# Optimization experiments

Measured on AMD Instinct MI355X. Metric: run time of the kernel, lower is better.

Reference implementation:

```python
import jax, jax.numpy as jnp
import numpy as np

B, T, H, D = 512, 256, 256, 3  # batch, seq_len, RNN_hid_dim, var_dim


def setup_inputs() -> dict:
    key = jax.random.key(0)
    ks = jax.random.split(key, 14)
    s = 1.0 / np.sqrt(H)  # PyTorch GRU init scale
    return {
        "X_p": jax.random.normal(ks[0], (B, T, D), jnp.float32),
        "X_f": jax.random.normal(ks[1], (B, T, D), jnp.float32),
        "noise": jax.random.normal(ks[2], (1, B, H), jnp.float32),
        # encoder GRU params (PyTorch layout: gates ordered r, z, n)
        "W_ih_enc": jax.random.uniform(ks[3], (3 * H, D), jnp.float32, -s, s),
        "W_hh_enc": jax.random.uniform(ks[4], (3 * H, H), jnp.float32, -s, s),
        "b_ih_enc": jax.random.uniform(ks[5], (3 * H,), jnp.float32, -s, s),
        "b_hh_enc": jax.random.uniform(ks[6], (3 * H,), jnp.float32, -s, s),
        # decoder GRU params
        "W_ih_dec": jax.random.uniform(ks[7], (3 * H, D), jnp.float32, -s, s),
        "W_hh_dec": jax.random.uniform(ks[8], (3 * H, H), jnp.float32, -s, s),
        "b_ih_dec": jax.random.uniform(ks[9], (3 * H,), jnp.float32, -s, s),
        "b_hh_dec": jax.random.uniform(ks[10], (3 * H,), jnp.float32, -s, s),
        # output projection
        "W_fc": jax.random.uniform(ks[11], (D, H), jnp.float32, -s, s),
        "b_fc": jax.random.uniform(ks[12], (D,), jnp.float32, -s, s),
    }


def _gru(x, h0, W_ih, W_hh, b_ih, b_hh):
    # x: [B, T, D]; h0: [B, H]. PyTorch GRU cell math, gate order r, z, n.
    xg = jnp.einsum('btd,gd->btg', x, W_ih) + b_ih  # [B, T, 3H] (one big GEMM)

    def step(h, xg_t):
        gh = h @ W_hh.T + b_hh                      # [B, 3H]
        xr, xz, xn = jnp.split(xg_t, 3, axis=-1)
        hr, hz, hn = jnp.split(gh, 3, axis=-1)
        r = jax.nn.sigmoid(xr + hr)
        z = jax.nn.sigmoid(xz + hz)
        n = jnp.tanh(xn + r * hn)
        h_new = (1.0 - z) * n + z * h
        return h_new, h_new

    hT, ys = jax.lax.scan(step, h0, jnp.swapaxes(xg, 0, 1))  # scan over T
    return jnp.swapaxes(ys, 0, 1), hT  # [B, T, H], [B, H]


def reference(X_p, X_f, noise, W_ih_enc, W_hh_enc, b_ih_enc, b_hh_enc,
              W_ih_dec, W_hh_dec, b_ih_dec, b_hh_dec, W_fc, b_fc):
    h0 = jnp.zeros((X_p.shape[0], W_hh_enc.shape[1]), X_p.dtype)
    _, h_t = _gru(X_p, h0, W_ih_enc, W_hh_enc, b_ih_enc, b_hh_enc)
    hidden = h_t + noise[0]                                   # h_t: [B,H], noise: [1,B,H]
    # shift right by one timestep, zero-fill first step
    X_f_shft = jnp.concatenate(
        [jnp.zeros_like(X_f[:, :1, :]), X_f[:, :-1, :]], axis=1)
    Y_f, _ = _gru(X_f_shft, hidden, W_ih_dec, W_hh_dec, b_ih_dec, b_hh_dec)
    return jnp.einsum('bth,dh->btd', Y_f, W_fc) + b_fc        # [B, T, D]
```

## Files before the change

### kernel.cpp

```cpp
#include <hip/hip_runtime.h>


#define B_TOT 512
#define T_LEN 256
#define HID 256
#define NBATCH 16
#define NTHREADS 1024
#define NBLK 32

#define WR_OFF 0
#define H_OFF  32768
#define X_OFF  40960
#define SMEM_SHORTS 57408
#define SMEM_BYTES  (SMEM_SHORTS * 2)

#define XT 64
#define XSLOTS (T_LEN + 1)
#define HBUF (NBATCH * HID)

typedef __attribute__((ext_vector_type(4))) float f32x4;
typedef __attribute__((ext_vector_type(8))) short shortx8;
typedef __attribute__((ext_vector_type(4))) short i16x4;
typedef __attribute__((ext_vector_type(4))) unsigned short ushortx4;
typedef __attribute__((ext_vector_type(8))) unsigned short ushortx8;

#if __has_builtin(__builtin_amdgcn_mfma_f32_16x16x16_bf16)
#define HAVE_K16 1
#define MFMA_X(A, B, C) __builtin_amdgcn_mfma_f32_16x16x16_bf16((A), (B), (C), 0, 0, 0)
#elif __has_builtin(__builtin_amdgcn_mfma_f32_16x16x16bf16_1k)
#define HAVE_K16 1
#define MFMA_X(A, B, C) __builtin_amdgcn_mfma_f32_16x16x16bf16_1k((A), (B), (C), 0, 0, 0)
#else
#define HAVE_K16 0
#endif

__device__ __forceinline__ unsigned short f2bf(float x) {
    unsigned u = __float_as_uint(x);
    u += 0x7FFF + ((u >> 16) & 1);
    return (unsigned short)(u >> 16);
}
__device__ __forceinline__ float bf2f(unsigned short s) {
    return __uint_as_float(((unsigned)s) << 16);
}
__device__ __forceinline__ float fastrcp(float x) {
#if __has_builtin(__builtin_amdgcn_rcpf)
    return __builtin_amdgcn_rcpf(x);
#else
    return 1.0f / x;
#endif
}
__device__ __forceinline__ float exp2raw(float y) {
#if __has_builtin(__builtin_amdgcn_exp2f)
    return __builtin_amdgcn_exp2f(y);
#else
    return __expf(y * 0.69314718056f);
#endif
}
__device__ __forceinline__ float sigmoid_(float x) {
    return fastrcp(1.0f + exp2raw(x * -1.44269504f));
}
__device__ __forceinline__ float tanh_(float x) {
    return 2.0f * fastrcp(1.0f + exp2raw(x * -2.88539008f)) - 1.0f;
}

__global__ __launch_bounds__(256) void prep_wr(
    const float* __restrict__ Whh_enc, const float* __restrict__ Whh_dec,
    unsigned short* __restrict__ wr_enc, unsigned short* __restrict__ wr_dec)
{
    int idx = blockIdx.x * 256 + threadIdx.x;
    int gru = idx >> 12;
    int rem = idx & 4095;
    int lane = rem & 63;
    int kk = (rem >> 6) & 3;
    int ht = rem >> 8;
    const float* W = gru ? Whh_dec : Whh_enc;
    unsigned short* dst = gru ? wr_dec : wr_enc;
    int row = ht * 16 + (lane & 15);
    int col = (kk + 4) * 32 + (lane >> 4) * 8;
    const float* src = W + (size_t)row * 256 + col;
    ushortx8 v;
    #pragma unroll
    for (int j = 0; j < 8; ++j) v[j] = f2bf(src[j]);
    *(ushortx8*)(dst + (size_t)rem * 8) = v;
}

template<int IS_DEC>
__global__ __launch_bounds__(NTHREADS, 4) void gru_persistent(
    const float* __restrict__ X,
    const float* __restrict__ W_hh,
    const float* __restrict__ W_ih,
    const float* __restrict__ b_ih,
    const float* __restrict__ b_hh,
    const unsigned short* __restrict__ Wr4,
    const float* __restrict__ h_in,
    const float* __restrict__ noise,
    float* __restrict__ h_out,
    unsigned short* __restrict__ Yout)
{
    extern __shared__ unsigned short smem[];
    unsigned short* shWr = smem + WR_OFF;
    unsigned short* shH  = smem + H_OFF;
    unsigned short* shX  = smem + X_OFF;

    const int tid  = threadIdx.x;
    const int g    = blockIdx.x;
    const int w    = tid >> 6;
    const int lane = tid & 63;
    const int c    = lane & 15;
    const int q    = lane >> 4;
    const int ht   = w;

    for (int idx = tid; idx < NBATCH * XSLOTS; idx += NTHREADS) {
        int t = idx >> 4, cc = idx & 15;
        int ts = IS_DEC ? (t - 1) : t;
        float x0 = 0.0f, x1 = 0.0f, x2 = 0.0f;
        if (ts >= 0 && ts < T_LEN) {
            const float* xp = X + ((size_t)(g * NBATCH + cc) * T_LEN + ts) * 3;
            x0 = xp[0]; x1 = xp[1]; x2 = xp[2];
        }
        ushortx4 v = {f2bf(x0), f2bf(x1), f2bf(x2), (unsigned short)0x3F80};
        *(ushortx4*)&shX[t * XT + cc * 4] = v;
    }

    {
        int row = ht * 16 + c;
        const float* wp = W_hh + (size_t)row * 256 + q * 8;
        #pragma unroll
        for (int k = 0; k < 4; ++k) {
            const f32x4* p = (const f32x4*)(wp + k * 32);
            f32x4 f0 = p[0];
            f32x4 f1 = p[1];
            shortx8 a;
            a[0] = (short)f2bf(f0[0]); a[1] = (short)f2bf(f0[1]);
            a[2] = (short)f2bf(f0[2]); a[3] = (short)f2bf(f0[3]);
            a[4] = (short)f2bf(f1[0]); a[5] = (short)f2bf(f1[1]);
            a[6] = (short)f2bf(f1[2]); a[7] = (short)f2bf(f1[3]);
            *(shortx8*)&shWr[((ht * 4 + k) * 64 + lane) * 8] = a;
        }
    }

    shortx8 Wf[2][8];
    #pragma unroll
    for (int gg = 0; gg < 2; ++gg) {
        int row = (gg + 1) * 256 + ht * 16 + c;
        const float* wp = W_hh + (size_t)row * 256 + q * 8;
        #pragma unroll
        for (int k = 0; k < 8; ++k) {
            const f32x4* p = (const f32x4*)(wp + k * 32);
            f32x4 f0 = p[0];
            f32x4 f1 = p[1];
            shortx8 a;
            a[0] = (short)f2bf(f0[0]); a[1] = (short)f2bf(f0[1]);
            a[2] = (short)f2bf(f0[2]); a[3] = (short)f2bf(f0[3]);
            a[4] = (short)f2bf(f1[0]); a[5] = (short)f2bf(f1[1]);
            a[6] = (short)f2bf(f1[2]); a[7] = (short)f2bf(f1[3]);
            Wf[gg][k] = a;
        }
    }

#if HAVE_K16
    i16x4 ax[3];
#else
    shortx8 ax[3];
#endif
    {
        int rr_ = ht * 16 + c;
        int rowr = rr_, rowz = 256 + rr_, rown = 512 + rr_;
        short r0 = 0, r1 = 0, r2 = 0, r3 = 0, z0 = 0, z1 = 0, z2 = 0, z3 = 0;
        short n0 = 0, n1 = 0, n2 = 0, n3 = 0;
        if (q == 0) {
            r0 = (short)f2bf(W_ih[rowr * 3 + 0]);
            r1 = (short)f2bf(W_ih[rowr * 3 + 1]);
            r2 = (short)f2bf(W_ih[rowr * 3 + 2]);
            r3 = (short)f2bf(b_ih[rowr] + b_hh[rowr]);
            z0 = (short)f2bf(W_ih[rowz * 3 + 0]);
            z1 = (short)f2bf(W_ih[rowz * 3 + 1]);
            z2 = (short)f2bf(W_ih[rowz * 3 + 2]);
            z3 = (short)f2bf(b_ih[rowz] + b_hh[rowz]);
            n0 = (short)f2bf(W_ih[rown * 3 + 0]);
            n1 = (short)f2bf(W_ih[rown * 3 + 1]);
            n2 = (short)f2bf(W_ih[rown * 3 + 2]);
            n3 = (short)f2bf(b_ih[rown]);
        }
#if HAVE_K16
        ax[0] = i16x4{r0, r1, r2, r3};
        ax[1] = i16x4{z0, z1, z2, z3};
        ax[2] = i16x4{n0, n1, n2, n3};
#else
        ax[0] = shortx8{r0, r1, r2, r3, 0, 0, 0, 0};
        ax[1] = shortx8{z0, z1, z2, z3, 0, 0, 0, 0};
        ax[2] = shortx8{n0, n1, n2, n3, 0, 0, 0, 0};
#endif
    }

    f32x4 nhb = *(const f32x4*)(b_hh + 512 + ht * 16 + q * 4);

    int woff;
    {
        int kk = ht >> 1;
        int qq = ((ht & 1) << 1) | (q >> 1);
        woff = ((kk * 4 + qq) * 16 + c) * 8 + (q & 1) * 4;
    }

    f32x4 hold = {0.0f, 0.0f, 0.0f, 0.0f};
    if (IS_DEC) {
        int b = g * NBATCH + c;
        int dim0 = ht * 16 + q * 4;
        f32x4 h0 = *(const f32x4*)(h_in + (size_t)b * HID + dim0);
        f32x4 nz = *(const f32x4*)(noise + (size_t)b * HID + dim0);
        hold = h0 + nz;
    }
    {
        ushortx4 hb16 = {f2bf(hold[0]), f2bf(hold[1]), f2bf(hold[2]), f2bf(hold[3])};
        *(ushortx4*)&shH[woff] = hb16;
    }

    unsigned short* yp = nullptr;
    if (IS_DEC)
        yp = Yout + ((size_t)g * T_LEN * NBATCH + c) * HID + ht * 16 + q * 4;

    __syncthreads();

    const f32x4 zc = {0.0f, 0.0f, 0.0f, 0.0f};

    f32x4 acc0, acc1, acc2, acc3;
    {
#if HAVE_K16
        i16x4 bx = *(const i16x4*)&shX[c * 4];
        acc0 = MFMA_X(ax[0], bx, zc);
        acc1 = MFMA_X(ax[1], bx, zc);
        acc3 = MFMA_X(ax[2], bx, zc);
#else
        ushortx4 xv = *(const ushortx4*)&shX[c * 4];
        shortx8 bx = (q == 0)
            ? shortx8{(short)xv[0], (short)xv[1], (short)xv[2], (short)xv[3], 0, 0, 0, 0}
            : shortx8{0, 0, 0, 0, 0, 0, 0, 0};
        acc0 = __builtin_amdgcn_mfma_f32_16x16x32_bf16(ax[0], bx, zc, 0, 0, 0);
        acc1 = __builtin_amdgcn_mfma_f32_16x16x32_bf16(ax[1], bx, zc, 0, 0, 0);
        acc3 = __builtin_amdgcn_mfma_f32_16x16x32_bf16(ax[2], bx, zc, 0, 0, 0);
#endif
    }

    const int bbase = q * 128 + c * 8;
    const unsigned short* ab = shWr + ((size_t)(ht * 4) * 64 + lane) * 8;
    const unsigned short* gb = Wr4 + ((size_t)(ht * 4) * 64 + lane) * 8;

    int xidx = XT + c * 4;

    for (int t = 0; t < T_LEN; ++t) {
        const unsigned short* brow = shH + (t & 1) * HBUF + bbase;
        unsigned short* hn = shH + ((t + 1) & 1) * HBUF;

        shortx8 gr[4];
        #pragma unroll
        for (int kk = 0; kk < 4; ++kk)
            gr[kk] = *(const shortx8*)(gb + kk * 512);

        acc2 = nhb;

        #pragma unroll
        for (int k = 0; k < 4; ++k) {
            shortx8 bf = *(const shortx8*)(brow + k * 512);
            shortx8 ar = *(const shortx8*)(ab + k * 512);
            acc0 = __builtin_amdgcn_mfma_f32_16x16x32_bf16(ar,       bf, acc0, 0, 0, 0);
            acc1 = __builtin_amdgcn_mfma_f32_16x16x32_bf16(Wf[0][k], bf, acc1, 0, 0, 0);
            acc2 = __builtin_amdgcn_mfma_f32_16x16x32_bf16(Wf[1][k], bf, acc2, 0, 0, 0);
        }
        #pragma unroll
        for (int k = 4; k < 8; ++k) {
            shortx8 bf = *(const shortx8*)(brow + k * 512);
            acc0 = __builtin_amdgcn_mfma_f32_16x16x32_bf16(gr[k - 4], bf, acc0, 0, 0, 0);
            acc1 = __builtin_amdgcn_mfma_f32_16x16x32_bf16(Wf[0][k],  bf, acc1, 0, 0, 0);
            acc2 = __builtin_amdgcn_mfma_f32_16x16x32_bf16(Wf[1][k],  bf, acc2, 0, 0, 0);
        }

#if HAVE_K16
        i16x4 bxn = *(const i16x4*)&shX[xidx];
#else
        ushortx4 xvn = *(const ushortx4*)&shX[xidx];
        shortx8 bxn = (q == 0)
            ? shortx8{(short)xvn[0], (short)xvn[1], (short)xvn[2], (short)xvn[3], 0, 0, 0, 0}
            : shortx8{0, 0, 0, 0, 0, 0, 0, 0};
#endif
        xidx += XT;

        f32x4 ho;
        #pragma unroll
        for (int r = 0; r < 4; ++r) {
            float rr = sigmoid_(acc0[r]);
            float zz = sigmoid_(acc1[r]);
            float nn = tanh_(acc3[r] + rr * acc2[r]);
            ho[r] = nn + zz * (hold[r] - nn);
        }
        hold = ho;
        ushortx4 hb16 = {f2bf(ho[0]), f2bf(ho[1]), f2bf(ho[2]), f2bf(ho[3])};
        *(ushortx4*)(hn + woff) = hb16;
        if (IS_DEC) {
            *(ushortx4*)yp = hb16;
            yp += NBATCH * HID;
        }

#if HAVE_K16
        acc0 = MFMA_X(ax[0], bxn, zc);
        acc1 = MFMA_X(ax[1], bxn, zc);
        acc3 = MFMA_X(ax[2], bxn, zc);
#else
        acc0 = __builtin_amdgcn_mfma_f32_16x16x32_bf16(ax[0], bxn, zc, 0, 0, 0);
        acc1 = __builtin_amdgcn_mfma_f32_16x16x32_bf16(ax[1], bxn, zc, 0, 0, 0);
        acc3 = __builtin_amdgcn_mfma_f32_16x16x32_bf16(ax[2], bxn, zc, 0, 0, 0);
#endif
        __syncthreads();
    }

    if (!IS_DEC) {
        int dim0 = ht * 16 + q * 4;
        *(f32x4*)(h_out + (size_t)(g * NBATCH + c) * HID + dim0) = hold;
    }
}

__global__ __launch_bounds__(256) void proj_kernel(
    const unsigned short* __restrict__ Y, const float* __restrict__ W_fc,
    const float* __restrict__ b_fc, float* __restrict__ out)
{
    int row = blockIdx.x * 256 + threadIdx.x;
    int b16 = row & 15;
    int gt = row >> 4;
    int t = gt & (T_LEN - 1);
    int g = gt >> 8;
    const unsigned short* y = Y + (size_t)row * HID;
    float a0 = b_fc[0], a1 = b_fc[1], a2 = b_fc[2];
    #pragma unroll 4
    for (int k8 = 0; k8 < 32; ++k8) {
        ushortx8 v = *(const ushortx8*)(y + k8 * 8);
        #pragma unroll
        for (int j = 0; j < 8; ++j) {
            float f = bf2f(v[j]);
            int k = k8 * 8 + j;
            a0 += f * W_fc[k];
            a1 += f * W_fc[256 + k];
            a2 += f * W_fc[512 + k];
        }
    }
    int batch = g * NBATCH + b16;
    float* o = out + ((size_t)batch * T_LEN + t) * 3;
    o[0] = a0; o[1] = a1; o[2] = a2;
}

extern "C" void kernel_launch(void* const* d_in, const int* in_sizes, int n_in,
                              void* d_out, int out_size, void* d_ws, size_t ws_size,
                              hipStream_t stream)
{
    const float* X_p      = (const float*)d_in[0];
    const float* X_f      = (const float*)d_in[1];
    const float* noise    = (const float*)d_in[2];
    const float* W_ih_enc = (const float*)d_in[3];
    const float* W_hh_enc = (const float*)d_in[4];
    const float* b_ih_enc = (const float*)d_in[5];
    const float* b_hh_enc = (const float*)d_in[6];
    const float* W_ih_dec = (const float*)d_in[7];
    const float* W_hh_dec = (const float*)d_in[8];
    const float* b_ih_dec = (const float*)d_in[9];
    const float* b_hh_dec = (const float*)d_in[10];
    const float* W_fc     = (const float*)d_in[11];
    const float* b_fc     = (const float*)d_in[12];

    (void)hipFuncSetAttribute((const void*)&gru_persistent<0>,
                              hipFuncAttributeMaxDynamicSharedMemorySize, SMEM_BYTES);
    (void)hipFuncSetAttribute((const void*)&gru_persistent<1>,
                              hipFuncAttributeMaxDynamicSharedMemorySize, SMEM_BYTES);

    float* h_enc = (float*)d_ws;
    unsigned short* wr_enc = (unsigned short*)((char*)d_ws + (512u << 10));
    unsigned short* wr_dec = (unsigned short*)((char*)d_ws + (576u << 10));
    unsigned short* Yws    = (unsigned short*)((char*)d_ws + (640u << 10));

    hipLaunchKernelGGL(prep_wr, dim3(32), dim3(256), 0, stream,
        W_hh_enc, W_hh_dec, wr_enc, wr_dec);

    hipLaunchKernelGGL((gru_persistent<0>), dim3(NBLK), dim3(NTHREADS), SMEM_BYTES, stream,
        X_p, W_hh_enc, W_ih_enc, b_ih_enc, b_hh_enc, wr_enc,
        (const float*)nullptr, (const float*)nullptr, h_enc,
        (unsigned short*)nullptr);

    hipLaunchKernelGGL((gru_persistent<1>), dim3(NBLK), dim3(NTHREADS), SMEM_BYTES, stream,
        X_f, W_hh_dec, W_ih_dec, b_ih_dec, b_hh_dec, wr_dec,
        h_enc, noise, (float*)nullptr, Yws);

    hipLaunchKernelGGL(proj_kernel, dim3((B_TOT * T_LEN) / 256), dim3(256), 0, stream,
        Yws, W_fc, b_fc, (float*)d_out);
}
```

Baseline: 806.8 us.

## Split batch across more blocks with 4 real rows per block and LDS gate redistribution

Each persistent GRU block now handles only 4 batch rows instead of 16, so the launch uses 128 blocks rather than 32 and the serial recurrence is spread across more CUs. The MFMA tiles stay 16 wide with 12 rows zero-padded. Gate accumulators are staged through a new LDS region so each lane runs the nonlinearity for a single (batch, hidden) element, cutting per-lane transcendental work fourfold. The cost is extra LDS writes and reads per step, three quarters of the MFMA work wasted on padding, and larger shared memory per block.

```diff
diff --git a/kernel.cpp b/kernel.cpp
--- a/kernel.cpp
+++ b/kernel.cpp
@@ -5,13 +5,15 @@
 #define T_LEN 256
 #define HID 256
 #define NBATCH 16
+#define NB 4
 #define NTHREADS 1024
-#define NBLK 32
+#define NBLK (B_TOT / NB)
 
 #define WR_OFF 0
 #define H_OFF  32768
 #define X_OFF  40960
-#define SMEM_SHORTS 57408
+#define RD_OFF 57408
+#define SMEM_SHORTS (RD_OFF + 16 * 512)
 #define SMEM_BYTES  (SMEM_SHORTS * 2)
 
 #define XT 64
@@ -101,6 +103,7 @@
     unsigned short* shWr = smem + WR_OFF;
     unsigned short* shH  = smem + H_OFF;
     unsigned short* shX  = smem + X_OFF;
+    unsigned short* shRd = smem + RD_OFF;
 
     const int tid  = threadIdx.x;
     const int g    = blockIdx.x;
@@ -109,13 +112,16 @@
     const int c    = lane & 15;
     const int q    = lane >> 4;
     const int ht   = w;
+    const int cv   = lane >> 4;
+    const int din  = lane & 15;
+    const int d_glob = ht * 16 + din;
 
     for (int idx = tid; idx < NBATCH * XSLOTS; idx += NTHREADS) {
         int t = idx >> 4, cc = idx & 15;
         int ts = IS_DEC ? (t - 1) : t;
         float x0 = 0.0f, x1 = 0.0f, x2 = 0.0f;
-        if (ts >= 0 && ts < T_LEN) {
-            const float* xp = X + ((size_t)(g * NBATCH + cc) * T_LEN + ts) * 3;
+        if (cc < NB && ts >= 0 && ts < T_LEN) {
+            const float* xp = X + ((size_t)(g * NB + cc) * T_LEN + ts) * 3;
             x0 = xp[0]; x1 = xp[1]; x2 = xp[2];
         }
         ushortx4 v = {f2bf(x0), f2bf(x1), f2bf(x2), (unsigned short)0x3F80};
@@ -195,29 +201,25 @@
 
     f32x4 nhb = *(const f32x4*)(b_hh + 512 + ht * 16 + q * 4);
 
-    int woff;
+    const int offv = ht * 256 + (din >> 3) * 128 + ((din >> 2) & 1) * 4
+                   + cv * 8 + (din & 3);
+
     {
-        int kk = ht >> 1;
-        int qq = ((ht & 1) << 1) | (q >> 1);
-        woff = ((kk * 4 + qq) * 16 + c) * 8 + (q & 1) * 4;
-    }
-
-    f32x4 hold = {0.0f, 0.0f, 0.0f, 0.0f};
+        const ushortx8 z8 = {0, 0, 0, 0, 0, 0, 0, 0};
+        *(ushortx8*)&shH[tid * 8] = z8;
+    }
+    __syncthreads();
+
+    float hold = 0.0f;
     if (IS_DEC) {
-        int b = g * NBATCH + c;
-        int dim0 = ht * 16 + q * 4;
-        f32x4 h0 = *(const f32x4*)(h_in + (size_t)b * HID + dim0);
-        f32x4 nz = *(const f32x4*)(noise + (size_t)b * HID + dim0);
-        hold = h0 + nz;
-    }
-    {
-        ushortx4 hb16 = {f2bf(hold[0]), f2bf(hold[1]), f2bf(hold[2]), f2bf(hold[3])};
-        *(ushortx4*)&shH[woff] = hb16;
+        int b = g * NB + cv;
+        hold = h_in[(size_t)b * HID + d_glob] + noise[(size_t)b * HID + d_glob];
+        shH[offv] = f2bf(hold);
     }
 
     unsigned short* yp = nullptr;
     if (IS_DEC)
-        yp = Yout + ((size_t)g * T_LEN * NBATCH + c) * HID + ht * 16 + q * 4;
+        yp = Yout + ((size_t)g * T_LEN * NB + cv) * HID + d_glob;
 
     __syncthreads();
 
@@ -244,6 +246,7 @@
     const int bbase = q * 128 + c * 8;
     const unsigned short* ab = shWr + ((size_t)(ht * 4) * 64 + lane) * 8;
     const unsigned short* gb = Wr4 + ((size_t)(ht * 4) * 64 + lane) * 8;
+    unsigned short* shRd_w = shRd + w * 512;
 
     int xidx = XT + c * 4;
 
@@ -274,6 +277,14 @@
             acc2 = __builtin_amdgcn_mfma_f32_16x16x32_bf16(Wf[1][k],  bf, acc2, 0, 0, 0);
         }
 
+        if (c < NB) {
+            #pragma unroll
+            for (int r = 0; r < 4; ++r) {
+                f32x4 v = {acc0[r], acc1[r], acc2[r], acc3[r]};
+                *(f32x4*)&shRd_w[(c * 16 + q * 4 + r) * 8] = v;
+            }
+        }
+
 #if HAVE_K16
         i16x4 bxn = *(const i16x4*)&shX[xidx];
 #else
@@ -284,22 +295,6 @@
 #endif
         xidx += XT;
 
-        f32x4 ho;
-        #pragma unroll
-        for (int r = 0; r < 4; ++r) {
-            float rr = sigmoid_(acc0[r]);
-            float zz = sigmoid_(acc1[r]);
-            float nn = tanh_(acc3[r] + rr * acc2[r]);
-            ho[r] = nn + zz * (hold[r] - nn);
-        }
-        hold = ho;
-        ushortx4 hb16 = {f2bf(ho[0]), f2bf(ho[1]), f2bf(ho[2]), f2bf(ho[3])};
-        *(ushortx4*)(hn + woff) = hb16;
-        if (IS_DEC) {
-            *(ushortx4*)yp = hb16;
-            yp += NBATCH * HID;
-        }
-
 #if HAVE_K16
         acc0 = MFMA_X(ax[0], bxn, zc);
         acc1 = MFMA_X(ax[1], bxn, zc);
@@ -309,12 +304,26 @@
         acc1 = __builtin_amdgcn_mfma_f32_16x16x32_bf16(ax[1], bxn, zc, 0, 0, 0);
         acc3 = __builtin_amdgcn_mfma_f32_16x16x32_bf16(ax[2], bxn, zc, 0, 0, 0);
 #endif
+
+        {
+            f32x4 av = *(const f32x4*)&shRd_w[lane * 8];
+            float rr = sigmoid_(av[0]);
+            float zz = sigmoid_(av[1]);
+            float nn = tanh_(av[3] + rr * av[2]);
+            float ho = nn + zz * (hold - nn);
+            hold = ho;
+            unsigned short hb = f2bf(ho);
+            hn[offv] = hb;
+            if (IS_DEC) {
+                *yp = hb;
+                yp += NB * HID;
+            }
+        }
         __syncthreads();
     }
 
     if (!IS_DEC) {
-        int dim0 = ht * 16 + q * 4;
-        *(f32x4*)(h_out + (size_t)(g * NBATCH + c) * HID + dim0) = hold;
+        h_out[(size_t)(g * NB + cv) * HID + d_glob] = hold;
     }
 }
 
@@ -323,8 +332,8 @@
     const float* __restrict__ b_fc, float* __restrict__ out)
 {
     int row = blockIdx.x * 256 + threadIdx.x;
-    int b16 = row & 15;
-    int gt = row >> 4;
+    int b4 = row & (NB - 1);
+    int gt = row >> 2;
     int t = gt & (T_LEN - 1);
     int g = gt >> 8;
     const unsigned short* y = Y + (size_t)row * HID;
@@ -341,7 +350,7 @@
             a2 += f * W_fc[512 + k];
         }
     }
-    int batch = g * NBATCH + b16;
+    int batch = g * NB + b4;
     float* o = out + ((size_t)batch * T_LEN + t) * 3;
     o[0] = a0; o[1] = a1; o[2] = a2;
 }
```

Measured after the change: 943.7 us. +17.0%, slower.

## Fuse encoder and decoder GRU into one persistent kernel

Applied to the files above, without the earlier changes.

Merges the two persistent GRU launches into a single kernel that runs the encoder phase and then the decoder phase in the same blocks. The final encoder hidden state stays in registers, so there is no global round trip through h_enc and one launch is removed. Both input sequences are staged into LDS up front, which enlarges the shared-memory footprint. Decoder outputs are now written with nontemporal stores, and launch bounds drop to a minimum of one block per CU.

```diff
diff --git a/kernel.cpp b/kernel.cpp
--- a/kernel.cpp
+++ b/kernel.cpp
@@ -8,15 +8,16 @@
 #define NTHREADS 1024
 #define NBLK 32
 
-#define WR_OFF 0
-#define H_OFF  32768
-#define X_OFF  40960
-#define SMEM_SHORTS 57408
-#define SMEM_BYTES  (SMEM_SHORTS * 2)
-
 #define XT 64
 #define XSLOTS (T_LEN + 1)
 #define HBUF (NBATCH * HID)
+
+#define WR_OFF 0
+#define H_OFF  32768
+#define X1_OFF 40960
+#define X2_OFF 57408
+#define SMEM_SHORTS (X2_OFF + XSLOTS * XT)
+#define SMEM_BYTES  (SMEM_SHORTS * 2)
 
 typedef __attribute__((ext_vector_type(4))) float f32x4;
 typedef __attribute__((ext_vector_type(8))) short shortx8;
@@ -84,23 +85,25 @@
     *(ushortx8*)(dst + (size_t)rem * 8) = v;
 }
 
-template<int IS_DEC>
-__global__ __launch_bounds__(NTHREADS, 4) void gru_persistent(
-    const float* __restrict__ X,
-    const float* __restrict__ W_hh,
-    const float* __restrict__ W_ih,
-    const float* __restrict__ b_ih,
-    const float* __restrict__ b_hh,
-    const unsigned short* __restrict__ Wr4,
-    const float* __restrict__ h_in,
+__global__ __launch_bounds__(NTHREADS, 1) void gru_fused(
+    const float* __restrict__ X_p,
+    const float* __restrict__ X_f,
+    const float* __restrict__ Whh_e,
+    const float* __restrict__ Whh_d,
+    const float* __restrict__ Wih_e,
+    const float* __restrict__ Wih_d,
+    const float* __restrict__ bih_e,
+    const float* __restrict__ bih_d,
+    const float* __restrict__ bhh_e,
+    const float* __restrict__ bhh_d,
+    const unsigned short* __restrict__ wr_e,
+    const unsigned short* __restrict__ wr_d,
     const float* __restrict__ noise,
-    float* __restrict__ h_out,
     unsigned short* __restrict__ Yout)
 {
     extern __shared__ unsigned short smem[];
     unsigned short* shWr = smem + WR_OFF;
     unsigned short* shH  = smem + H_OFF;
-    unsigned short* shX  = smem + X_OFF;
 
     const int tid  = threadIdx.x;
     const int g    = blockIdx.x;
@@ -110,90 +113,20 @@
     const int q    = lane >> 4;
     const int ht   = w;
 
-    for (int idx = tid; idx < NBATCH * XSLOTS; idx += NTHREADS) {
-        int t = idx >> 4, cc = idx & 15;
-        int ts = IS_DEC ? (t - 1) : t;
+    for (int idx = tid; idx < NBATCH * XSLOTS * 2; idx += NTHREADS) {
+        int half = idx >= NBATCH * XSLOTS;
+        int rem = half ? idx - NBATCH * XSLOTS : idx;
+        int t = rem >> 4, cc = rem & 15;
+        int ts = half ? (t - 1) : t;
+        const float* Xsrc = half ? X_f : X_p;
         float x0 = 0.0f, x1 = 0.0f, x2 = 0.0f;
         if (ts >= 0 && ts < T_LEN) {
-            const float* xp = X + ((size_t)(g * NBATCH + cc) * T_LEN + ts) * 3;
+            const float* xp = Xsrc + ((size_t)(g * NBATCH + cc) * T_LEN + ts) * 3;
             x0 = xp[0]; x1 = xp[1]; x2 = xp[2];
         }
         ushortx4 v = {f2bf(x0), f2bf(x1), f2bf(x2), (unsigned short)0x3F80};
-        *(ushortx4*)&shX[t * XT + cc * 4] = v;
+        *(ushortx4*)&smem[(half ? X2_OFF : X1_OFF) + t * XT + cc * 4] = v;
     }
-
-    {
-        int row = ht * 16 + c;
-        const float* wp = W_hh + (size_t)row * 256 + q * 8;
-        #pragma unroll
-        for (int k = 0; k < 4; ++k) {
-            const f32x4* p = (const f32x4*)(wp + k * 32);
-            f32x4 f0 = p[0];
-            f32x4 f1 = p[1];
-            shortx8 a;
-            a[0] = (short)f2bf(f0[0]); a[1] = (short)f2bf(f0[1]);
-            a[2] = (short)f2bf(f0[2]); a[3] = (short)f2bf(f0[3]);
-            a[4] = (short)f2bf(f1[0]); a[5] = (short)f2bf(f1[1]);
-            a[6] = (short)f2bf(f1[2]); a[7] = (short)f2bf(f1[3]);
-            *(shortx8*)&shWr[((ht * 4 + k) * 64 + lane) * 8] = a;
-        }
-    }
-
-    shortx8 Wf[2][8];
-    #pragma unroll
-    for (int gg = 0; gg < 2; ++gg) {
-        int row = (gg + 1) * 256 + ht * 16 + c;
-        const float* wp = W_hh + (size_t)row * 256 + q * 8;
-        #pragma unroll
-        for (int k = 0; k < 8; ++k) {
-            const f32x4* p = (const f32x4*)(wp + k * 32);
-            f32x4 f0 = p[0];
-            f32x4 f1 = p[1];
-            shortx8 a;
-            a[0] = (short)f2bf(f0[0]); a[1] = (short)f2bf(f0[1]);
-            a[2] = (short)f2bf(f0[2]); a[3] = (short)f2bf(f0[3]);
-            a[4] = (short)f2bf(f1[0]); a[5] = (short)f2bf(f1[1]);
-            a[6] = (short)f2bf(f1[2]); a[7] = (short)f2bf(f1[3]);
-            Wf[gg][k] = a;
-        }
-    }
-
-#if HAVE_K16
-    i16x4 ax[3];
-#else
-    shortx8 ax[3];
-#endif
-    {
-        int rr_ = ht * 16 + c;
-        int rowr = rr_, rowz = 256 + rr_, rown = 512 + rr_;
-        short r0 = 0, r1 = 0, r2 = 0, r3 = 0, z0 = 0, z1 = 0, z2 = 0, z3 = 0;
-        short n0 = 0, n1 = 0, n2 = 0, n3 = 0;
-        if (q == 0) {
-            r0 = (short)f2bf(W_ih[rowr * 3 + 0]);
-            r1 = (short)f2bf(W_ih[rowr * 3 + 1]);
-            r2 = (short)f2bf(W_ih[rowr * 3 + 2]);
-            r3 = (short)f2bf(b_ih[rowr] + b_hh[rowr]);
-            z0 = (short)f2bf(W_ih[rowz * 3 + 0]);
-            z1 = (short)f2bf(W_ih[rowz * 3 + 1]);
-            z2 = (short)f2bf(W_ih[rowz * 3 + 2]);
-            z3 = (short)f2bf(b_ih[rowz] + b_hh[rowz]);
-            n0 = (short)f2bf(W_ih[rown * 3 + 0]);
-            n1 = (short)f2bf(W_ih[rown * 3 + 1]);
-            n2 = (short)f2bf(W_ih[rown * 3 + 2]);
-            n3 = (short)f2bf(b_ih[rown]);
-        }
-#if HAVE_K16
-        ax[0] = i16x4{r0, r1, r2, r3};
-        ax[1] = i16x4{z0, z1, z2, z3};
-        ax[2] = i16x4{n0, n1, n2, n3};
-#else
-        ax[0] = shortx8{r0, r1, r2, r3, 0, 0, 0, 0};
-        ax[1] = shortx8{z0, z1, z2, z3, 0, 0, 0, 0};
-        ax[2] = shortx8{n0, n1, n2, n3, 0, 0, 0, 0};
-#endif
-    }
-
-    f32x4 nhb = *(const f32x4*)(b_hh + 512 + ht * 16 + q * 4);
 
     int woff;
     {
@@ -201,120 +134,205 @@
         int qq = ((ht & 1) << 1) | (q >> 1);
         woff = ((kk * 4 + qq) * 16 + c) * 8 + (q & 1) * 4;
     }
-
-    f32x4 hold = {0.0f, 0.0f, 0.0f, 0.0f};
-    if (IS_DEC) {
-        int b = g * NBATCH + c;
-        int dim0 = ht * 16 + q * 4;
-        f32x4 h0 = *(const f32x4*)(h_in + (size_t)b * HID + dim0);
-        f32x4 nz = *(const f32x4*)(noise + (size_t)b * HID + dim0);
-        hold = h0 + nz;
-    }
-    {
-        ushortx4 hb16 = {f2bf(hold[0]), f2bf(hold[1]), f2bf(hold[2]), f2bf(hold[3])};
-        *(ushortx4*)&shH[woff] = hb16;
-    }
-
-    unsigned short* yp = nullptr;
-    if (IS_DEC)
-        yp = Yout + ((size_t)g * T_LEN * NBATCH + c) * HID + ht * 16 + q * 4;
-
-    __syncthreads();
-
-    const f32x4 zc = {0.0f, 0.0f, 0.0f, 0.0f};
-
-    f32x4 acc0, acc1, acc2, acc3;
-    {
-#if HAVE_K16
-        i16x4 bx = *(const i16x4*)&shX[c * 4];
-        acc0 = MFMA_X(ax[0], bx, zc);
-        acc1 = MFMA_X(ax[1], bx, zc);
-        acc3 = MFMA_X(ax[2], bx, zc);
-#else
-        ushortx4 xv = *(const ushortx4*)&shX[c * 4];
-        shortx8 bx = (q == 0)
-            ? shortx8{(short)xv[0], (short)xv[1], (short)xv[2], (short)xv[3], 0, 0, 0, 0}
-            : shortx8{0, 0, 0, 0, 0, 0, 0, 0};
-        acc0 = __builtin_amdgcn_mfma_f32_16x16x32_bf16(ax[0], bx, zc, 0, 0, 0);
-        acc1 = __builtin_amdgcn_mfma_f32_16x16x32_bf16(ax[1], bx, zc, 0, 0, 0);
-        acc3 = __builtin_amdgcn_mfma_f32_16x16x32_bf16(ax[2], bx, zc, 0, 0, 0);
-#endif
-    }
-
     const int bbase = q * 128 + c * 8;
     const unsigned short* ab = shWr + ((size_t)(ht * 4) * 64 + lane) * 8;
-    const unsigned short* gb = Wr4 + ((size_t)(ht * 4) * 64 + lane) * 8;
-
-    int xidx = XT + c * 4;
-
-    for (int t = 0; t < T_LEN; ++t) {
-        const unsigned short* brow = shH + (t & 1) * HBUF + bbase;
-        unsigned short* hn = shH + ((t + 1) & 1) * HBUF;
-
-        shortx8 gr[4];
+    const f32x4 zc = {0.0f, 0.0f, 0.0f, 0.0f};
+
+    float hold0 = 0.0f, hold1 = 0.0f, hold2 = 0.0f, hold3 = 0.0f;
+
+    for (int phase = 0; phase < 2; ++phase) {
+        const float* W_hh = phase ? Whh_d : Whh_e;
+        const float* W_ih = phase ? Wih_d : Wih_e;
+        const float* b_ih = phase ? bih_d : bih_e;
+        const float* b_hh = phase ? bhh_d : bhh_e;
+        const unsigned short* Wr4 = phase ? wr_d : wr_e;
+        const unsigned short* shX = smem + (phase ? X2_OFF : X1_OFF);
+
+        __syncthreads();
+
+        {
+            int row = ht * 16 + c;
+            const float* wp = W_hh + (size_t)row * 256 + q * 8;
+            #pragma unroll
+            for (int k = 0; k < 4; ++k) {
+                const f32x4* p = (const f32x4*)(wp + k * 32);
+                f32x4 f0 = p[0];
+                f32x4 f1 = p[1];
+                shortx8 a;
+                a[0] = (short)f2bf(f0[0]); a[1] = (short)f2bf(f0[1]);
+                a[2] = (short)f2bf(f0[2]); a[3] = (short)f2bf(f0[3]);
+                a[4] = (short)f2bf(f1[0]); a[5] = (short)f2bf(f1[1]);
+                a[6] = (short)f2bf(f1[2]); a[7] = (short)f2bf(f1[3]);
+                *(shortx8*)&shWr[((ht * 4 + k) * 64 + lane) * 8] = a;
+            }
+        }
+
+        shortx8 Wf[2][8];
         #pragma unroll
-        for (int kk = 0; kk < 4; ++kk)
-            gr[kk] = *(const shortx8*)(gb + kk * 512);
-
-        acc2 = nhb;
-
-        #pragma unroll
-        for (int k = 0; k < 4; ++k) {
-            shortx8 bf = *(const shortx8*)(brow + k * 512);
-            shortx8 ar = *(const shortx8*)(ab + k * 512);
-            acc0 = __builtin_amdgcn_mfma_f32_16x16x32_bf16(ar,       bf, acc0, 0, 0, 0);
-            acc1 = __builtin_amdgcn_mfma_f32_16x16x32_bf16(Wf[0][k], bf, acc1, 0, 0, 0);
-            acc2 = __builtin_amdgcn_mfma_f32_16x16x32_bf16(Wf[1][k], bf, acc2, 0, 0, 0);
-        }
-        #pragma unroll
-        for (int k = 4; k < 8; ++k) {
-            shortx8 bf = *(const shortx8*)(brow + k * 512);
-            acc0 = __builtin_amdgcn_mfma_f32_16x16x32_bf16(gr[k - 4], bf, acc0, 0, 0, 0);
-            acc1 = __builtin_amdgcn_mfma_f32_16x16x32_bf16(Wf[0][k],  bf, acc1, 0, 0, 0);
-            acc2 = __builtin_amdgcn_mfma_f32_16x16x32_bf16(Wf[1][k],  bf, acc2, 0, 0, 0);
+        for (int gg = 0; gg < 2; ++gg) {
+            int row = (gg + 1) * 256 + ht * 16 + c;
+            const float* wp = W_hh + (size_t)row * 256 + q * 8;
+            #pragma unroll
+            for (int k = 0; k < 8; ++k) {
+                const f32x4* p = (const f32x4*)(wp + k * 32);
+                f32x4 f0 = p[0];
+                f32x4 f1 = p[1];
+                shortx8 a;
+                a[0] = (short)f2bf(f0[0]); a[1] = (short)f2bf(f0[1]);
+                a[2] = (short)f2bf(f0[2]); a[3] = (short)f2bf(f0[3]);
+                a[4] = (short)f2bf(f1[0]); a[5] = (short)f2bf(f1[1]);
+                a[6] = (short)f2bf(f1[2]); a[7] = (short)f2bf(f1[3]);
+                Wf[gg][k] = a;
+            }
         }
 
 #if HAVE_K16
-        i16x4 bxn = *(const i16x4*)&shX[xidx];
-#else
-        ushortx4 xvn = *(const ushortx4*)&shX[xidx];
-        shortx8 bxn = (q == 0)
-            ? shortx8{(short)xvn[0], (short)xvn[1], (short)xvn[2], (short)xvn[3], 0, 0, 0, 0}
-            : shortx8{0, 0, 0, 0, 0, 0, 0, 0};
-#endif
-        xidx += XT;
-
-        f32x4 ho;
-        #pragma unroll
-        for (int r = 0; r < 4; ++r) {
-            float rr = sigmoid_(acc0[r]);
-            float zz = sigmoid_(acc1[r]);
-            float nn = tanh_(acc3[r] + rr * acc2[r]);
-            ho[r] = nn + zz * (hold[r] - nn);
-        }
-        hold = ho;
-        ushortx4 hb16 = {f2bf(ho[0]), f2bf(ho[1]), f2bf(ho[2]), f2bf(ho[3])};
-        *(ushortx4*)(hn + woff) = hb16;
-        if (IS_DEC) {
-            *(ushortx4*)yp = hb16;
-            yp += NBATCH * HID;
-        }
-
+        i16x4 ax[3];
+#else
+        shortx8 ax[3];
+#endif
+        {
+            int rr_ = ht * 16 + c;
+            int rowr = rr_, rowz = 256 + rr_, rown = 512 + rr_;
+            short r0 = 0, r1 = 0, r2 = 0, r3 = 0, z0 = 0, z1 = 0, z2 = 0, z3 = 0;
+            short n0 = 0, n1 = 0, n2 = 0, n3 = 0;
+            if (q == 0) {
+                r0 = (short)f2bf(W_ih[rowr * 3 + 0]);
+                r1 = (short)f2bf(W_ih[rowr * 3 + 1]);
+                r2 = (short)f2bf(W_ih[rowr * 3 + 2]);
+                r3 = (short)f2bf(b_ih[rowr] + b_hh[rowr]);
+                z0 = (short)f2bf(W_ih[rowz * 3 + 0]);
+                z1 = (short)f2bf(W_ih[rowz * 3 + 1]);
+                z2 = (short)f2bf(W_ih[rowz * 3 + 2]);
+                z3 = (short)f2bf(b_ih[rowz] + b_hh[rowz]);
+                n0 = (short)f2bf(W_ih[rown * 3 + 0]);
+                n1 = (short)f2bf(W_ih[rown * 3 + 1]);
+                n2 = (short)f2bf(W_ih[rown * 3 + 2]);
+                n3 = (short)f2bf(b_ih[rown]);
+            }
 #if HAVE_K16
-        acc0 = MFMA_X(ax[0], bxn, zc);
-        acc1 = MFMA_X(ax[1], bxn, zc);
-        acc3 = MFMA_X(ax[2], bxn, zc);
-#else
-        acc0 = __builtin_amdgcn_mfma_f32_16x16x32_bf16(ax[0], bxn, zc, 0, 0, 0);
-        acc1 = __builtin_amdgcn_mfma_f32_16x16x32_bf16(ax[1], bxn, zc, 0, 0, 0);
-        acc3 = __builtin_amdgcn_mfma_f32_16x16x32_bf16(ax[2], bxn, zc, 0, 0, 0);
-#endif
+            ax[0] = i16x4{r0, r1, r2, r3};
+            ax[1] = i16x4{z0, z1, z2, z3};
+            ax[2] = i16x4{n0, n1, n2, n3};
+#else
+            ax[0] = shortx8{r0, r1, r2, r3, 0, 0, 0, 0};
+            ax[1] = shortx8{z0, z1, z2, z3, 0, 0, 0, 0};
+            ax[2] = shortx8{n0, n1, n2, n3, 0, 0, 0, 0};
+#endif
+        }
+
+        f32x4 nhb = *(const f32x4*)(b_hh + 512 + ht * 16 + q * 4);
+
+        if (phase == 0) {
+            hold0 = hold1 = hold2 = hold3 = 0.0f;
+        } else {
+            int b = g * NBATCH + c;
+            int dim0 = ht * 16 + q * 4;
+            f32x4 nz = *(const f32x4*)(noise + (size_t)b * HID + dim0);
+            hold0 += nz[0]; hold1 += nz[1]; hold2 += nz[2]; hold3 += nz[3];
+        }
+        {
+            ushortx4 hb16 = {f2bf(hold0), f2bf(hold1), f2bf(hold2), f2bf(hold3)};
+            *(ushortx4*)&shH[woff] = hb16;
+        }
+
+        unsigned short* yp = Yout + ((size_t)g * T_LEN * NBATCH + c) * HID
+                           + ht * 16 + q * 4;
+
+        const unsigned short* gb = Wr4 + ((size_t)(ht * 4) * 64 + lane) * 8;
+
         __syncthreads();
-    }
-
-    if (!IS_DEC) {
-        int dim0 = ht * 16 + q * 4;
-        *(f32x4*)(h_out + (size_t)(g * NBATCH + c) * HID + dim0) = hold;
+
+        f32x4 acc0, acc1, acc2, acc3;
+        {
+#if HAVE_K16
+            i16x4 bx = *(const i16x4*)&shX[c * 4];
+            acc0 = MFMA_X(ax[0], bx, zc);
+            acc1 = MFMA_X(ax[1], bx, zc);
+            acc3 = MFMA_X(ax[2], bx, zc);
+#else
+            ushortx4 xv = *(const ushortx4*)&shX[c * 4];
+            shortx8 bx = (q == 0)
+                ? shortx8{(short)xv[0], (short)xv[1], (short)xv[2], (short)xv[3], 0, 0, 0, 0}
+                : shortx8{0, 0, 0, 0, 0, 0, 0, 0};
+            acc0 = __builtin_amdgcn_mfma_f32_16x16x32_bf16(ax[0], bx, zc, 0, 0, 0);
+            acc1 = __builtin_amdgcn_mfma_f32_16x16x32_bf16(ax[1], bx, zc, 0, 0, 0);
+            acc3 = __builtin_amdgcn_mfma_f32_16x16x32_bf16(ax[2], bx, zc, 0, 0, 0);
+#endif
+        }
+
+        int xidx = XT + c * 4;
+
+        for (int t = 0; t < T_LEN; ++t) {
+            const unsigned short* brow = shH + (t & 1) * HBUF + bbase;
+            unsigned short* hn = shH + ((t + 1) & 1) * HBUF;
+
+            shortx8 gr[4];
+            #pragma unroll
+            for (int kk = 0; kk < 4; ++kk)
+                gr[kk] = *(const shortx8*)(gb + kk * 512);
+
+            acc2 = nhb;
+
+            #pragma unroll
+            for (int k = 0; k < 4; ++k) {
+                shortx8 bf = *(const shortx8*)(brow + k * 512);
+                shortx8 ar = *(const shortx8*)(ab + k * 512);
+                acc0 = __builtin_amdgcn_mfma_f32_16x16x32_bf16(ar,       bf, acc0, 0, 0, 0);
+                acc1 = __builtin_amdgcn_mfma_f32_16x16x32_bf16(Wf[0][k], bf, acc1, 0, 0, 0);
+                acc2 = __builtin_amdgcn_mfma_f32_16x16x32_bf16(Wf[1][k], bf, acc2, 0, 0, 0);
+            }
+            #pragma unroll
+            for (int k = 4; k < 8; ++k) {
+                shortx8 bf = *(const shortx8*)(brow + k * 512);
+                acc0 = __builtin_amdgcn_mfma_f32_16x16x32_bf16(gr[k - 4], bf, acc0, 0, 0, 0);
+                acc1 = __builtin_amdgcn_mfma_f32_16x16x32_bf16(Wf[0][k],  bf, acc1, 0, 0, 0);
+                acc2 = __builtin_amdgcn_mfma_f32_16x16x32_bf16(Wf[1][k],  bf, acc2, 0, 0, 0);
+            }
+
+#if HAVE_K16
+            i16x4 bxn = *(const i16x4*)&shX[xidx];
+#else
+            ushortx4 xvn = *(const ushortx4*)&shX[xidx];
+            shortx8 bxn = (q == 0)
+                ? shortx8{(short)xvn[0], (short)xvn[1], (short)xvn[2], (short)xvn[3], 0, 0, 0, 0}
+                : shortx8{0, 0, 0, 0, 0, 0, 0, 0};
+#endif
+            xidx += XT;
+
+            {
+                float rr, zz, nn;
+                rr = sigmoid_(acc0[0]); zz = sigmoid_(acc1[0]);
+                nn = tanh_(acc3[0] + rr * acc2[0]);
+                hold0 = nn + zz * (hold0 - nn);
+                rr = sigmoid_(acc0[1]); zz = sigmoid_(acc1[1]);
+                nn = tanh_(acc3[1] + rr * acc2[1]);
+                hold1 = nn + zz * (hold1 - nn);
+                rr = sigmoid_(acc0[2]); zz = sigmoid_(acc1[2]);
+                nn = tanh_(acc3[2] + rr * acc2[2]);
+                hold2 = nn + zz * (hold2 - nn);
+                rr = sigmoid_(acc0[3]); zz = sigmoid_(acc1[3]);
+                nn = tanh_(acc3[3] + rr * acc2[3]);
+                hold3 = nn + zz * (hold3 - nn);
+                ushortx4 hb16 = {f2bf(hold0), f2bf(hold1), f2bf(hold2), f2bf(hold3)};
+                *(ushortx4*)(hn + woff) = hb16;
+                if (phase) {
+                    __builtin_nontemporal_store(hb16, (ushortx4*)yp);
+                    yp += NBATCH * HID;
+                }
+            }
+
+#if HAVE_K16
+            acc0 = MFMA_X(ax[0], bxn, zc);
+            acc1 = MFMA_X(ax[1], bxn, zc);
+            acc3 = MFMA_X(ax[2], bxn, zc);
+#else
+            acc0 = __builtin_amdgcn_mfma_f32_16x16x32_bf16(ax[0], bxn, zc, 0, 0, 0);
+            acc1 = __builtin_amdgcn_mfma_f32_16x16x32_bf16(ax[1], bxn, zc, 0, 0, 0);
+            acc3 = __builtin_amdgcn_mfma_f32_16x16x32_bf16(ax[2], bxn, zc, 0, 0, 0);
+#endif
+            __syncthreads();
+        }
     }
 }
 
@@ -364,27 +382,20 @@
     const float* W_fc     = (const float*)d_in[11];
     const float* b_fc     = (const float*)d_in[12];
 
-    (void)hipFuncSetAttribute((const void*)&gru_persistent<0>,
+    (void)hipFuncSetAttribute((const void*)&gru_fused,
                               hipFuncAttributeMaxDynamicSharedMemorySize, SMEM_BYTES);
-    (void)hipFuncSetAttribute((const void*)&gru_persistent<1>,
-                              hipFuncAttributeMaxDynamicSharedMemorySize, SMEM_BYTES);
-
-    float* h_enc = (float*)d_ws;
-    unsigned short* wr_enc = (unsigned short*)((char*)d_ws + (512u << 10));
-    unsigned short* wr_dec = (unsigned short*)((char*)d_ws + (576u << 10));
-    unsigned short* Yws    = (unsigned short*)((char*)d_ws + (640u << 10));
+
+    unsigned short* wr_enc = (unsigned short*)d_ws;
+    unsigned short* wr_dec = (unsigned short*)((char*)d_ws + (64u << 10));
+    unsigned short* Yws    = (unsigned short*)((char*)d_ws + (128u << 10));
 
     hipLaunchKernelGGL(prep_wr, dim3(32), dim3(256), 0, stream,
         W_hh_enc, W_hh_dec, wr_enc, wr_dec);
 
-    hipLaunchKernelGGL((gru_persistent<0>), dim3(NBLK), dim3(NTHREADS), SMEM_BYTES, stream,
-        X_p, W_hh_enc, W_ih_enc, b_ih_enc, b_hh_enc, wr_enc,
-        (const float*)nullptr, (const float*)nullptr, h_enc,
-        (unsigned short*)nullptr);
-
-    hipLaunchKernelGGL((gru_persistent<1>), dim3(NBLK), dim3(NTHREADS), SMEM_BYTES, stream,
-        X_f, W_hh_dec, W_ih_dec, b_ih_dec, b_hh_dec, wr_dec,
-        h_enc, noise, (float*)nullptr, Yws);
+    hipLaunchKernelGGL(gru_fused, dim3(NBLK), dim3(NTHREADS), SMEM_BYTES, stream,
+        X_p, X_f, W_hh_enc, W_hh_dec, W_ih_enc, W_ih_dec,
+        b_ih_enc, b_ih_dec, b_hh_enc, b_hh_dec,
+        wr_enc, wr_dec, noise, Yws);
 
     hipLaunchKernelGGL(proj_kernel, dim3((B_TOT * T_LEN) / 256), dim3(256), 0, stream,
         Yws, W_fc, b_fc, (float*)d_out);
```

Result: no change. 813.3 us (+0.8%).
